# Kernel tuning notes

Measured on AMD Instinct MI355X. Metric: run time of the kernel, lower is better.

Reference implementation:

```python
import jax, jax.numpy as jnp
import numpy as np

B, T, D, H = 8, 1024, 1024, 16
HD = D // H  # head_dim = 64


def setup_inputs() -> dict:
    key = jax.random.key(0)
    ks = jax.random.split(key, 3)
    scale = 0.02
    return {
        "x": jax.random.normal(ks[0], (B, T, D), dtype=jnp.float32),
        "w_qkv": jax.random.normal(ks[1], (D, 3 * D), dtype=jnp.float32) * scale,
        "b_qkv": jnp.zeros((3 * D,), dtype=jnp.float32),
        "w_proj": jax.random.normal(ks[2], (D, D), dtype=jnp.float32) * scale,
        "b_proj": jnp.zeros((D,), dtype=jnp.float32),
    }


def reference(x, w_qkv, b_qkv, w_proj, b_proj):
    b, t, c = x.shape
    qkv = x @ w_qkv + b_qkv                      # [B,T,3D]
    qkv = qkv.reshape(b, t, 3, H, HD)
    q, k, v = [jnp.transpose(qkv[:, :, i], (0, 2, 1, 3)) for i in range(3)]  # [B,H,T,HD]
    att = jnp.einsum("bhqd,bhkd->bhqk", q, k) / np.sqrt(HD)
    causal = jnp.triu(jnp.ones((t, t), dtype=bool), k=1)
    att = jnp.where(causal, -jnp.inf, att)
    att = jax.nn.softmax(att, axis=-1)
    out = jnp.einsum("bhqk,bhkd->bhqd", att, v)  # [B,H,T,HD]
    out = jnp.transpose(out, (0, 2, 1, 3)).reshape(b, t, c)
    return out @ w_proj + b_proj
```

## Files before the change

### kernel.cpp

```cpp
#include <hip/hip_runtime.h>
#include <hip/hip_bf16.h>

#define BATCH 8
#define SEQ   1024
#define DIM   1024
#define NH    16
#define HDIM  64
#define LDQKV 3072

typedef __attribute__((ext_vector_type(8))) short bf16x8;
typedef __attribute__((ext_vector_type(4))) float f32x4;

typedef const __attribute__((address_space(1))) void* gvptr;
typedef __attribute__((address_space(3))) void* lvptr;

static __device__ __forceinline__ short f2bf(float f) {
    unsigned u = __float_as_uint(f);
    unsigned r = (u + 0x7fffu + ((u >> 16) & 1u)) >> 16;
    return (short)r;
}
static __device__ __forceinline__ unsigned pack2bf(float lo, float hi) {
    unsigned a = __float_as_uint(lo), b = __float_as_uint(hi);
    return ((a + 0x8000u) >> 16) | ((b + 0x8000u) & 0xffff0000u);
}

__global__ __launch_bounds__(256) void cast_f2b_kernel(
    const float* __restrict__ in, short* __restrict__ out)
{
    size_t i = ((size_t)blockIdx.x * 256 + threadIdx.x) * 8;
    float4 a = *(const float4*)&in[i];
    float4 b = *(const float4*)&in[i + 4];
    bf16x8 o;
    o[0] = f2bf(a.x); o[1] = f2bf(a.y); o[2] = f2bf(a.z); o[3] = f2bf(a.w);
    o[4] = f2bf(b.x); o[5] = f2bf(b.y); o[6] = f2bf(b.z); o[7] = f2bf(b.w);
    *(bf16x8*)&out[i] = o;
}

__global__ __launch_bounds__(256) void tcast_kernel(
    const float* __restrict__ in, short* __restrict__ out, int R, int C)
{
    __shared__ float Ld[32][33];
    const int tx = threadIdx.x & 31;
    const int ty = threadIdx.x >> 5;
    const int c0 = blockIdx.x * 32;
    const int r0 = blockIdx.y * 32;
#pragma unroll
    for (int i = 0; i < 4; i++) {
        int r = ty + i * 8;
        Ld[r][tx] = in[(size_t)(r0 + r) * C + c0 + tx];
    }
    __syncthreads();
#pragma unroll
    for (int i = 0; i < 4; i++) {
        int rr = ty + i * 8;
        out[(size_t)(c0 + rr) * R + r0 + tx] = f2bf(Ld[tx][rr]);
    }
}

#define GBM 128
#define GBN 256
#define GBK 64
#define NKT (DIM / GBK)
#define SLOT_SH (GBM * GBK + GBN * GBK)

static __device__ __forceinline__ void stage_tile(
    const short* __restrict__ A, const short* __restrict__ Bt,
    short* sb, int m0, int n0, int kt, int tid)
{
#pragma unroll
    for (int r = 0; r < 2; r++) {
        int off16 = tid + r * 512;
        int row   = off16 >> 3;
        int s     = (off16 & 7) ^ (row & 7);
        __builtin_amdgcn_global_load_lds(
            (gvptr)&A[(size_t)(m0 + row) * DIM + kt + s * 8],
            (lvptr)&sb[off16 * 8], 16, 0, 0);
    }
    short* bb = sb + GBM * GBK;
#pragma unroll
    for (int r = 0; r < 4; r++) {
        int off16 = tid + r * 512;
        int row   = off16 >> 3;
        int s     = (off16 & 7) ^ (row & 7);
        __builtin_amdgcn_global_load_lds(
            (gvptr)&Bt[(size_t)(n0 + row) * DIM + kt + s * 8],
            (lvptr)&bb[off16 * 8], 16, 0, 0);
    }
}

template<bool OUT_BF16>
__global__ __launch_bounds__(512, 2) void gemm_pipe_kernel(
    const short* __restrict__ A,
    const short* __restrict__ Bt,
    const float* __restrict__ bias,
    void* __restrict__ Cout,
    int N)
{
    __shared__ __align__(16) short lds[3 * SLOT_SH];

    const int tid  = threadIdx.x;
    const int lane = tid & 63;
    const int l16  = lane & 15;
    const int quad = lane >> 4;
    const int w    = tid >> 6;
    const int wm   = w >> 2;
    const int wn   = w & 3;
    const int m0   = blockIdx.y * GBM;
    const int n0   = blockIdx.x * GBN;

    f32x4 acc[4][4];
#pragma unroll
    for (int mi = 0; mi < 4; mi++)
#pragma unroll
        for (int ni = 0; ni < 4; ni++) acc[mi][ni] = (f32x4){0.f, 0.f, 0.f, 0.f};

    stage_tile(A, Bt, &lds[0],         m0, n0, 0,   tid);
    stage_tile(A, Bt, &lds[SLOT_SH],   m0, n0, GBK, tid);
    asm volatile("s_waitcnt vmcnt(6) lgkmcnt(0)\n\ts_barrier" ::: "memory");

#pragma unroll
    for (int t = 0; t < NKT; t++) {
        if (t + 2 < NKT)
            stage_tile(A, Bt, &lds[((t + 2) % 3) * SLOT_SH],
                       m0, n0, (t + 2) * GBK, tid);

        const short* ab = &lds[(t % 3) * SLOT_SH];
        const short* bb = ab + GBM * GBK;

        bf16x8 af[4][2], bfr[4][2];
#pragma unroll
        for (int mi = 0; mi < 4; mi++) {
            int row = wm * 64 + mi * 16 + l16;
#pragma unroll
            for (int ks = 0; ks < 2; ks++)
                af[mi][ks] = *(const bf16x8*)
                    &ab[row * GBK + (((ks * 4 + quad) ^ (row & 7)) * 8)];
        }
#pragma unroll
        for (int ni = 0; ni < 4; ni++) {
            int row = wn * 64 + ni * 16 + l16;
#pragma unroll
            for (int ks = 0; ks < 2; ks++)
                bfr[ni][ks] = *(const bf16x8*)
                    &bb[row * GBK + (((ks * 4 + quad) ^ (row & 7)) * 8)];
        }

        __builtin_amdgcn_s_setprio(1);
#pragma unroll
        for (int ks = 0; ks < 2; ks++)
#pragma unroll
            for (int mi = 0; mi < 4; mi++)
#pragma unroll
                for (int ni = 0; ni < 4; ni++)
                    acc[mi][ni] = __builtin_amdgcn_mfma_f32_16x16x32_bf16(
                        af[mi][ks], bfr[ni][ks], acc[mi][ni], 0, 0, 0);
        __builtin_amdgcn_s_setprio(0);

        if (t < NKT - 2)
            asm volatile("s_waitcnt vmcnt(6) lgkmcnt(0)\n\ts_barrier" ::: "memory");
        else if (t < NKT - 1)
            asm volatile("s_waitcnt vmcnt(0) lgkmcnt(0)\n\ts_barrier" ::: "memory");
    }

#pragma unroll
    for (int ni = 0; ni < 4; ni++) {
        int n = n0 + wn * 64 + ni * 16 + l16;
        float bv = bias[n];
#pragma unroll
        for (int mi = 0; mi < 4; mi++) {
#pragma unroll
            for (int reg = 0; reg < 4; reg++) {
                int m = m0 + wm * 64 + mi * 16 + quad * 4 + reg;
                float v = acc[mi][ni][reg] + bv;
                if (OUT_BF16)
                    ((short*)Cout)[(size_t)m * N + n] = f2bf(v);
                else
                    ((float*)Cout)[(size_t)m * N + n] = v;
            }
        }
    }
}

#define LDK 72
#define LDP 72

__global__ __launch_bounds__(256, 4) void attn_kernel(
    const short* __restrict__ qkv, short* __restrict__ out)
{
    const int bh    = blockIdx.x;
    const int qtile = 7 - (int)blockIdx.y;
    const int b  = bh >> 4;
    const int h  = bh & 15;
    const int q0 = qtile * 128;
    const int tid  = threadIdx.x;
    const int w    = tid >> 6;
    const int lane = tid & 63;
    const int l16  = lane & 15;
    const int quad = lane >> 4;

    __shared__ __align__(16) short Ks[64 * LDK];
    __shared__ __align__(16) short Vt[64 * LDK];
    __shared__ __align__(16) short QP[128 * LDP];

    const short* qbase = qkv + (size_t)(b * SEQ + q0) * LDQKV + h * HDIM;
#pragma unroll
    for (int s = 0; s < 4; s++) {
        int vi = tid + s * 256;
        int row = vi >> 3, d8 = (vi & 7) * 8;
        *(bf16x8*)&QP[row * LDP + d8] =
            *(const bf16x8*)&qbase[(size_t)row * LDQKV + d8];
    }
    __syncthreads();

    bf16x8 qfragT[2][2];
#pragma unroll
    for (int qb = 0; qb < 2; qb++)
#pragma unroll
        for (int ks = 0; ks < 2; ks++)
            qfragT[qb][ks] = *(const bf16x8*)
                &QP[(w * 32 + qb * 16 + l16) * LDP + ks * 32 + quad * 8];

    f32x4 o_accT[2][4];
#pragma unroll
    for (int qb = 0; qb < 2; qb++)
#pragma unroll
        for (int db = 0; db < 4; db++) o_accT[qb][db] = (f32x4){0.f, 0.f, 0.f, 0.f};
    float l_run[2] = {0.f, 0.f};

    const int nkt = 2 * qtile + 2;
    const short* kb0 = qkv + (size_t)b * SEQ * LDQKV + DIM + h * HDIM;
    const short* vb0 = kb0 + DIM;

    const int vkey0 = (tid & 15) * 4;
    const int vd4   = (tid >> 4) * 4;

    bf16x8 kreg[2];
    short4 vreg[4];
#pragma unroll
    for (int s = 0; s < 2; s++) {
        int vi = tid + s * 256;
        kreg[s] = *(const bf16x8*)&kb0[(size_t)(vi >> 3) * LDQKV + (vi & 7) * 8];
    }
#pragma unroll
    for (int i = 0; i < 4; i++)
        vreg[i] = *(const short4*)&vb0[(size_t)(vkey0 + i) * LDQKV + vd4];
#pragma unroll
    for (int s = 0; s < 2; s++) {
        int vi = tid + s * 256;
        *(bf16x8*)&Ks[(vi >> 3) * LDK + (vi & 7) * 8] = kreg[s];
    }
    *(short4*)&Vt[(vd4 + 0) * LDK + vkey0] = make_short4(vreg[0].x, vreg[1].x, vreg[2].x, vreg[3].x);
    *(short4*)&Vt[(vd4 + 1) * LDK + vkey0] = make_short4(vreg[0].y, vreg[1].y, vreg[2].y, vreg[3].y);
    *(short4*)&Vt[(vd4 + 2) * LDK + vkey0] = make_short4(vreg[0].z, vreg[1].z, vreg[2].z, vreg[3].z);
    *(short4*)&Vt[(vd4 + 3) * LDK + vkey0] = make_short4(vreg[0].w, vreg[1].w, vreg[2].w, vreg[3].w);

    for (int kt = 0; kt < nkt; kt++) {
        __syncthreads();
        const int k0 = kt * 64;

        if (kt + 1 < nkt) {
            const short* kb = kb0 + (size_t)(k0 + 64) * LDQKV;
            const short* vb = vb0 + (size_t)(k0 + 64) * LDQKV;
#pragma unroll
            for (int s = 0; s < 2; s++) {
                int vi = tid + s * 256;
                kreg[s] = *(const bf16x8*)&kb[(size_t)(vi >> 3) * LDQKV + (vi & 7) * 8];
            }
#pragma unroll
            for (int i = 0; i < 4; i++)
                vreg[i] = *(const short4*)&vb[(size_t)(vkey0 + i) * LDQKV + vd4];
        }

        f32x4 sT[2][4];
#pragma unroll
        for (int qb = 0; qb < 2; qb++)
#pragma unroll
            for (int kb = 0; kb < 4; kb++) sT[qb][kb] = (f32x4){0.f, 0.f, 0.f, 0.f};
#pragma unroll
        for (int kb = 0; kb < 4; kb++) {
            bf16x8 kf0 = *(const bf16x8*)&Ks[(kb * 16 + l16) * LDK + quad * 8];
            bf16x8 kf1 = *(const bf16x8*)&Ks[(kb * 16 + l16) * LDK + 32 + quad * 8];
#pragma unroll
            for (int qb = 0; qb < 2; qb++) {
                sT[qb][kb] = __builtin_amdgcn_mfma_f32_16x16x32_bf16(
                    kf0, qfragT[qb][0], sT[qb][kb], 0, 0, 0);
                sT[qb][kb] = __builtin_amdgcn_mfma_f32_16x16x32_bf16(
                    kf1, qfragT[qb][1], sT[qb][kb], 0, 0, 0);
            }
        }

        const bool domask = (kt >= nkt - 2);
#pragma unroll
        for (int qb = 0; qb < 2; qb++) {
            const int q = q0 + w * 32 + qb * 16 + l16;
            float lsum = 0.f;
#pragma unroll
            for (int kb = 0; kb < 4; kb++) {
                float p[4];
#pragma unroll
                for (int r = 0; r < 4; r++) {
                    float e = __expf(sT[qb][kb][r] * 0.125f);
                    int key = k0 + kb * 16 + quad * 4 + r;
                    p[r] = (!domask || key <= q) ? e : 0.f;
                    lsum += p[r];
                }
                unsigned d0 = pack2bf(p[0], p[1]);
                unsigned d1 = pack2bf(p[2], p[3]);
                *(uint2*)&QP[(w * 32 + qb * 16 + l16) * LDP + kb * 16 + quad * 4] =
                    make_uint2(d0, d1);
            }
            lsum += __shfl_xor(lsum, 16, 64);
            lsum += __shfl_xor(lsum, 32, 64);
            l_run[qb] += lsum;
        }

#pragma unroll
        for (int ks2 = 0; ks2 < 2; ks2++) {
            bf16x8 pf[2];
#pragma unroll
            for (int qb = 0; qb < 2; qb++)
                pf[qb] = *(const bf16x8*)
                    &QP[(w * 32 + qb * 16 + l16) * LDP + ks2 * 32 + quad * 8];
#pragma unroll
            for (int db = 0; db < 4; db++) {
                bf16x8 vf = *(const bf16x8*)&Vt[(db * 16 + l16) * LDK + ks2 * 32 + quad * 8];
#pragma unroll
                for (int qb = 0; qb < 2; qb++)
                    o_accT[qb][db] = __builtin_amdgcn_mfma_f32_16x16x32_bf16(
                        vf, pf[qb], o_accT[qb][db], 0, 0, 0);
            }
        }

        __syncthreads();
        if (kt + 1 < nkt) {
#pragma unroll
            for (int s = 0; s < 2; s++) {
                int vi = tid + s * 256;
                *(bf16x8*)&Ks[(vi >> 3) * LDK + (vi & 7) * 8] = kreg[s];
            }
            *(short4*)&Vt[(vd4 + 0) * LDK + vkey0] = make_short4(vreg[0].x, vreg[1].x, vreg[2].x, vreg[3].x);
            *(short4*)&Vt[(vd4 + 1) * LDK + vkey0] = make_short4(vreg[0].y, vreg[1].y, vreg[2].y, vreg[3].y);
            *(short4*)&Vt[(vd4 + 2) * LDK + vkey0] = make_short4(vreg[0].z, vreg[1].z, vreg[2].z, vreg[3].z);
            *(short4*)&Vt[(vd4 + 3) * LDK + vkey0] = make_short4(vreg[0].w, vreg[1].w, vreg[2].w, vreg[3].w);
        }
    }

#pragma unroll
    for (int qb = 0; qb < 2; qb++) {
        const float inv = 1.f / l_run[qb];
        const int q = q0 + w * 32 + qb * 16 + l16;
        short* ob = out + (size_t)(b * SEQ + q) * DIM + h * HDIM;
#pragma unroll
        for (int db = 0; db < 4; db++) {
            float v0 = o_accT[qb][db][0] * inv;
            float v1 = o_accT[qb][db][1] * inv;
            float v2 = o_accT[qb][db][2] * inv;
            float v3 = o_accT[qb][db][3] * inv;
            *(uint2*)&ob[db * 16 + quad * 4] =
                make_uint2(pack2bf(v0, v1), pack2bf(v2, v3));
        }
    }
}

extern "C" void kernel_launch(void* const* d_in, const int* in_sizes, int n_in,
                              void* d_out, int out_size, void* d_ws, size_t ws_size,
                              hipStream_t stream)
{
    const float* x      = (const float*)d_in[0];
    const float* w_qkv  = (const float*)d_in[1];
    const float* b_qkv  = (const float*)d_in[2];
    const float* w_proj = (const float*)d_in[3];
    const float* b_proj = (const float*)d_in[4];
    float* out = (float*)d_out;

    const int M = BATCH * SEQ;

    short* xb    = (short*)d_ws;
    short* wqb   = xb   + (size_t)M * DIM;
    short* wpb   = wqb  + (size_t)LDQKV * DIM;
    short* qkvb  = wpb  + (size_t)DIM * DIM;
    short* attnb = qkvb + (size_t)M * LDQKV;

    cast_f2b_kernel<<<(M * DIM) / (256 * 8), 256, 0, stream>>>(x, xb);
    tcast_kernel<<<dim3(LDQKV / 32, DIM / 32), 256, 0, stream>>>(w_qkv, wqb, DIM, LDQKV);
    tcast_kernel<<<dim3(DIM / 32, DIM / 32), 256, 0, stream>>>(w_proj, wpb, DIM, DIM);

    gemm_pipe_kernel<true><<<dim3(LDQKV / GBN, M / GBM), 512, 0, stream>>>(
        xb, wqb, b_qkv, (void*)qkvb, LDQKV);

    attn_kernel<<<dim3(BATCH * NH, SEQ / 128), 256, 0, stream>>>(qkvb, attnb);

    gemm_pipe_kernel<false><<<dim3(DIM / GBN, M / GBM), 512, 0, stream>>>(
        attnb, wpb, b_proj, (void*)out, DIM);
}
```

Measured before the change: 219.6 us.

## Replace triple-buffered GEMM with double-buffered 256-row tiles and per-GEMM N widths

The GEMM kernel moves from 128x256 tiles with a three-slot LDS pipeline to 256xBN tiles with two LDS buffers and plain __syncthreads between phases. The QKV projection uses BN=192 (16x32=512 blocks) and the output projection uses BN=128 (8x32=256 blocks), each warp now holding 8xNFR accumulators. The aim is more operand reuse per LDS load and better grid sizing for each GEMM. In exchange it adds register pressure (up to 8x3 f32x4 accumulators plus fragments) and drops the finer vmcnt-based overlap, relying on coarser barriers.

After: 224.0 us. +2.0%, slower.

```diff
diff --git a/kernel.cpp b/kernel.cpp
--- a/kernel.cpp
+++ b/kernel.cpp
@@ -57,46 +57,45 @@
     }
 }
 
-#define GBM 128
-#define GBN 256
-#define GBK 64
-#define NKT (DIM / GBK)
-#define SLOT_SH (GBM * GBK + GBN * GBK)
-
-static __device__ __forceinline__ void stage_tile(
+#define GK 1024
+
+template<int BN>
+static __device__ __forceinline__ void stage_tile_db(
     const short* __restrict__ A, const short* __restrict__ Bt,
     short* sb, int m0, int n0, int kt, int tid)
 {
-#pragma unroll
-    for (int r = 0; r < 2; r++) {
-        int off16 = tid + r * 512;
-        int row   = off16 >> 3;
-        int s     = (off16 & 7) ^ (row & 7);
-        __builtin_amdgcn_global_load_lds(
-            (gvptr)&A[(size_t)(m0 + row) * DIM + kt + s * 8],
-            (lvptr)&sb[off16 * 8], 16, 0, 0);
-    }
-    short* bb = sb + GBM * GBK;
 #pragma unroll
     for (int r = 0; r < 4; r++) {
         int off16 = tid + r * 512;
         int row   = off16 >> 3;
         int s     = (off16 & 7) ^ (row & 7);
         __builtin_amdgcn_global_load_lds(
-            (gvptr)&Bt[(size_t)(n0 + row) * DIM + kt + s * 8],
+            (gvptr)&A[(size_t)(m0 + row) * GK + kt + s * 8],
+            (lvptr)&sb[off16 * 8], 16, 0, 0);
+    }
+    short* bb = sb + 256 * 64;
+#pragma unroll
+    for (int r = 0; r < BN / 64; r++) {
+        int off16 = tid + r * 512;
+        int row   = off16 >> 3;
+        int s     = (off16 & 7) ^ (row & 7);
+        __builtin_amdgcn_global_load_lds(
+            (gvptr)&Bt[(size_t)(n0 + row) * GK + kt + s * 8],
             (lvptr)&bb[off16 * 8], 16, 0, 0);
     }
 }
 
-template<bool OUT_BF16>
-__global__ __launch_bounds__(512, 2) void gemm_pipe_kernel(
+template<int BN, bool OUT_BF16>
+__global__ __launch_bounds__(512, 2) void gemm_db_kernel(
     const short* __restrict__ A,
     const short* __restrict__ Bt,
     const float* __restrict__ bias,
     void* __restrict__ Cout,
     int N)
 {
-    __shared__ __align__(16) short lds[3 * SLOT_SH];
+    constexpr int NFR  = BN / 64;
+    constexpr int SLOT = 256 * 64 + BN * 64;
+    __shared__ __align__(16) short lds[2 * SLOT];
 
     const int tid  = threadIdx.x;
     const int lane = tid & 63;
@@ -105,72 +104,96 @@
     const int w    = tid >> 6;
     const int wm   = w >> 2;
     const int wn   = w & 3;
-    const int m0   = blockIdx.y * GBM;
-    const int n0   = blockIdx.x * GBN;
-
-    f32x4 acc[4][4];
-#pragma unroll
-    for (int mi = 0; mi < 4; mi++)
-#pragma unroll
-        for (int ni = 0; ni < 4; ni++) acc[mi][ni] = (f32x4){0.f, 0.f, 0.f, 0.f};
-
-    stage_tile(A, Bt, &lds[0],         m0, n0, 0,   tid);
-    stage_tile(A, Bt, &lds[SLOT_SH],   m0, n0, GBK, tid);
-    asm volatile("s_waitcnt vmcnt(6) lgkmcnt(0)\n\ts_barrier" ::: "memory");
-
-#pragma unroll
-    for (int t = 0; t < NKT; t++) {
-        if (t + 2 < NKT)
-            stage_tile(A, Bt, &lds[((t + 2) % 3) * SLOT_SH],
-                       m0, n0, (t + 2) * GBK, tid);
-
-        const short* ab = &lds[(t % 3) * SLOT_SH];
-        const short* bb = ab + GBM * GBK;
-
-        bf16x8 af[4][2], bfr[4][2];
-#pragma unroll
-        for (int mi = 0; mi < 4; mi++) {
-            int row = wm * 64 + mi * 16 + l16;
-#pragma unroll
-            for (int ks = 0; ks < 2; ks++)
-                af[mi][ks] = *(const bf16x8*)
-                    &ab[row * GBK + (((ks * 4 + quad) ^ (row & 7)) * 8)];
-        }
-#pragma unroll
-        for (int ni = 0; ni < 4; ni++) {
-            int row = wn * 64 + ni * 16 + l16;
-#pragma unroll
-            for (int ks = 0; ks < 2; ks++)
-                bfr[ni][ks] = *(const bf16x8*)
-                    &bb[row * GBK + (((ks * 4 + quad) ^ (row & 7)) * 8)];
-        }
-
-        __builtin_amdgcn_s_setprio(1);
-#pragma unroll
-        for (int ks = 0; ks < 2; ks++)
-#pragma unroll
-            for (int mi = 0; mi < 4; mi++)
-#pragma unroll
-                for (int ni = 0; ni < 4; ni++)
-                    acc[mi][ni] = __builtin_amdgcn_mfma_f32_16x16x32_bf16(
-                        af[mi][ks], bfr[ni][ks], acc[mi][ni], 0, 0, 0);
-        __builtin_amdgcn_s_setprio(0);
-
-        if (t < NKT - 2)
-            asm volatile("s_waitcnt vmcnt(6) lgkmcnt(0)\n\ts_barrier" ::: "memory");
-        else if (t < NKT - 1)
-            asm volatile("s_waitcnt vmcnt(0) lgkmcnt(0)\n\ts_barrier" ::: "memory");
-    }
-
-#pragma unroll
-    for (int ni = 0; ni < 4; ni++) {
-        int n = n0 + wn * 64 + ni * 16 + l16;
+    const int m0   = blockIdx.y * 256;
+    const int n0   = blockIdx.x * BN;
+
+    f32x4 acc[8][NFR];
+#pragma unroll
+    for (int mi = 0; mi < 8; mi++)
+#pragma unroll
+        for (int ni = 0; ni < NFR; ni++) acc[mi][ni] = (f32x4){0.f, 0.f, 0.f, 0.f};
+
+    stage_tile_db<BN>(A, Bt, &lds[0], m0, n0, 0, tid);
+    __syncthreads();
+
+    for (int t2 = 0; t2 < 8; t2++) {
+        const int ta = 2 * t2;
+        const int tb = 2 * t2 + 1;
+
+        stage_tile_db<BN>(A, Bt, &lds[SLOT], m0, n0, (ta + 1) * 64, tid);
+        {
+            const short* ab = &lds[0];
+            const short* bb = ab + 256 * 64;
+#pragma unroll
+            for (int ks = 0; ks < 2; ks++) {
+                bf16x8 af[8], bfr[NFR];
+#pragma unroll
+                for (int mi = 0; mi < 8; mi++) {
+                    int row = wm * 128 + mi * 16 + l16;
+                    af[mi] = *(const bf16x8*)
+                        &ab[row * 64 + (((ks * 4 + quad) ^ (row & 7)) * 8)];
+                }
+#pragma unroll
+                for (int ni = 0; ni < NFR; ni++) {
+                    int row = wn * (BN / 4) + ni * 16 + l16;
+                    bfr[ni] = *(const bf16x8*)
+                        &bb[row * 64 + (((ks * 4 + quad) ^ (row & 7)) * 8)];
+                }
+                __builtin_amdgcn_s_setprio(1);
+#pragma unroll
+                for (int mi = 0; mi < 8; mi++)
+#pragma unroll
+                    for (int ni = 0; ni < NFR; ni++)
+                        acc[mi][ni] = __builtin_amdgcn_mfma_f32_16x16x32_bf16(
+                            af[mi], bfr[ni], acc[mi][ni], 0, 0, 0);
+                __builtin_amdgcn_s_setprio(0);
+            }
+        }
+        __syncthreads();
+
+        if (t2 < 7)
+            stage_tile_db<BN>(A, Bt, &lds[0], m0, n0, (tb + 1) * 64, tid);
+        {
+            const short* ab = &lds[SLOT];
+            const short* bb = ab + 256 * 64;
+#pragma unroll
+            for (int ks = 0; ks < 2; ks++) {
+                bf16x8 af[8], bfr[NFR];
+#pragma unroll
+                for (int mi = 0; mi < 8; mi++) {
+                    int row = wm * 128 + mi * 16 + l16;
+                    af[mi] = *(const bf16x8*)
+                        &ab[row * 64 + (((ks * 4 + quad) ^ (row & 7)) * 8)];
+                }
+#pragma unroll
+                for (int ni = 0; ni < NFR; ni++) {
+                    int row = wn * (BN / 4) + ni * 16 + l16;
+                    bfr[ni] = *(const bf16x8*)
+                        &bb[row * 64 + (((ks * 4 + quad) ^ (row & 7)) * 8)];
+                }
+                __builtin_amdgcn_s_setprio(1);
+#pragma unroll
+                for (int mi = 0; mi < 8; mi++)
+#pragma unroll
+                    for (int ni = 0; ni < NFR; ni++)
+                        acc[mi][ni] = __builtin_amdgcn_mfma_f32_16x16x32_bf16(
+                            af[mi], bfr[ni], acc[mi][ni], 0, 0, 0);
+                __builtin_amdgcn_s_setprio(0);
+            }
+        }
+        if (t2 < 7)
+            __syncthreads();
+    }
+
+#pragma unroll
+    for (int ni = 0; ni < NFR; ni++) {
+        int n = n0 + wn * (BN / 4) + ni * 16 + l16;
         float bv = bias[n];
 #pragma unroll
-        for (int mi = 0; mi < 4; mi++) {
+        for (int mi = 0; mi < 8; mi++) {
 #pragma unroll
             for (int reg = 0; reg < 4; reg++) {
-                int m = m0 + wm * 64 + mi * 16 + quad * 4 + reg;
+                int m = m0 + wm * 128 + mi * 16 + quad * 4 + reg;
                 float v = acc[mi][ni][reg] + bv;
                 if (OUT_BF16)
                     ((short*)Cout)[(size_t)m * N + n] = f2bf(v);
@@ -385,11 +408,11 @@
     tcast_kernel<<<dim3(LDQKV / 32, DIM / 32), 256, 0, stream>>>(w_qkv, wqb, DIM, LDQKV);
     tcast_kernel<<<dim3(DIM / 32, DIM / 32), 256, 0, stream>>>(w_proj, wpb, DIM, DIM);
 
-    gemm_pipe_kernel<true><<<dim3(LDQKV / GBN, M / GBM), 512, 0, stream>>>(
+    gemm_db_kernel<192, true><<<dim3(LDQKV / 192, M / 256), 512, 0, stream>>>(
         xb, wqb, b_qkv, (void*)qkvb, LDQKV);
 
     attn_kernel<<<dim3(BATCH * NH, SEQ / 128), 256, 0, stream>>>(qkvb, attnb);
 
-    gemm_pipe_kernel<false><<<dim3(DIM / GBN, M / GBM), 512, 0, stream>>>(
+    gemm_db_kernel<128, false><<<dim3(DIM / 128, M / 256), 512, 0, stream>>>(
         attnb, wpb, b_proj, (void*)out, DIM);
 }
```

## Split GEMM k-step into two half-phases interleaving A/B staging with MFMA

Applied to the files above, without the earlier changes.

Restructures the GEMM main loop into two sub-phases per k-tile. Each phase loads half the fragments (ks=0 then ks=1), issues the A or B global-to-LDS staging for tile t+2, then runs MFMAs between extra barriers. The intent is to overlap global loads and LDS reads with matrix math more finely, in the style of a ping-pong schedule. The cost is more barriers per iteration, and the split of vmcnt accounting between A and B loads needs to stay correct.

New measurement: 220.1 us. Within noise of the previous version (+0.2%).

```diff
diff --git a/kernel.cpp b/kernel.cpp
--- a/kernel.cpp
+++ b/kernel.cpp
@@ -60,12 +60,12 @@
 #define GBM 128
 #define GBN 256
 #define GBK 64
-#define NKT (DIM / GBK)
+#define GK  1024
+#define NKT (GK / GBK)
 #define SLOT_SH (GBM * GBK + GBN * GBK)
 
-static __device__ __forceinline__ void stage_tile(
-    const short* __restrict__ A, const short* __restrict__ Bt,
-    short* sb, int m0, int n0, int kt, int tid)
+static __device__ __forceinline__ void stage_A(
+    const short* __restrict__ A, short* sb, int m0, int kt, int tid)
 {
 #pragma unroll
     for (int r = 0; r < 2; r++) {
@@ -73,18 +73,22 @@
         int row   = off16 >> 3;
         int s     = (off16 & 7) ^ (row & 7);
         __builtin_amdgcn_global_load_lds(
-            (gvptr)&A[(size_t)(m0 + row) * DIM + kt + s * 8],
+            (gvptr)&A[(size_t)(m0 + row) * GK + kt + s * 8],
             (lvptr)&sb[off16 * 8], 16, 0, 0);
     }
-    short* bb = sb + GBM * GBK;
+}
+
+static __device__ __forceinline__ void stage_B(
+    const short* __restrict__ Bt, short* bbuf, int n0, int kt, int tid)
+{
 #pragma unroll
     for (int r = 0; r < 4; r++) {
         int off16 = tid + r * 512;
         int row   = off16 >> 3;
         int s     = (off16 & 7) ^ (row & 7);
         __builtin_amdgcn_global_load_lds(
-            (gvptr)&Bt[(size_t)(n0 + row) * DIM + kt + s * 8],
-            (lvptr)&bb[off16 * 8], 16, 0, 0);
+            (gvptr)&Bt[(size_t)(n0 + row) * GK + kt + s * 8],
+            (lvptr)&bbuf[off16 * 8], 16, 0, 0);
     }
 }
 
@@ -114,52 +118,75 @@
 #pragma unroll
         for (int ni = 0; ni < 4; ni++) acc[mi][ni] = (f32x4){0.f, 0.f, 0.f, 0.f};
 
-    stage_tile(A, Bt, &lds[0],         m0, n0, 0,   tid);
-    stage_tile(A, Bt, &lds[SLOT_SH],   m0, n0, GBK, tid);
-    asm volatile("s_waitcnt vmcnt(6) lgkmcnt(0)\n\ts_barrier" ::: "memory");
+    stage_A(A, &lds[0], m0, 0, tid);
+    stage_B(Bt, &lds[0] + GBM * GBK, n0, 0, tid);
+    stage_A(A, &lds[SLOT_SH], m0, GBK, tid);
+    stage_B(Bt, &lds[SLOT_SH] + GBM * GBK, n0, GBK, tid);
+    asm volatile("s_waitcnt vmcnt(6) lgkmcnt(0)" ::: "memory");
+    __builtin_amdgcn_s_barrier();
 
 #pragma unroll
     for (int t = 0; t < NKT; t++) {
-        if (t + 2 < NKT)
-            stage_tile(A, Bt, &lds[((t + 2) % 3) * SLOT_SH],
-                       m0, n0, (t + 2) * GBK, tid);
-
         const short* ab = &lds[(t % 3) * SLOT_SH];
         const short* bb = ab + GBM * GBK;
-
-        bf16x8 af[4][2], bfr[4][2];
+        short* sb = &lds[((t + 2) % 3) * SLOT_SH];
+        const int kt2 = (t + 2) * GBK;
+
+        bf16x8 af0[4], bf0[4];
 #pragma unroll
         for (int mi = 0; mi < 4; mi++) {
             int row = wm * 64 + mi * 16 + l16;
-#pragma unroll
-            for (int ks = 0; ks < 2; ks++)
-                af[mi][ks] = *(const bf16x8*)
-                    &ab[row * GBK + (((ks * 4 + quad) ^ (row & 7)) * 8)];
+            af0[mi] = *(const bf16x8*)
+                &ab[row * GBK + ((quad ^ (row & 7)) * 8)];
         }
 #pragma unroll
         for (int ni = 0; ni < 4; ni++) {
             int row = wn * 64 + ni * 16 + l16;
-#pragma unroll
-            for (int ks = 0; ks < 2; ks++)
-                bfr[ni][ks] = *(const bf16x8*)
-                    &bb[row * GBK + (((ks * 4 + quad) ^ (row & 7)) * 8)];
-        }
-
+            bf0[ni] = *(const bf16x8*)
+                &bb[row * GBK + ((quad ^ (row & 7)) * 8)];
+        }
+        if (t + 2 < NKT) stage_A(A, sb, m0, kt2, tid);
+        __builtin_amdgcn_s_barrier();
+        asm volatile("s_waitcnt lgkmcnt(0)" ::: "memory");
         __builtin_amdgcn_s_setprio(1);
 #pragma unroll
-        for (int ks = 0; ks < 2; ks++)
-#pragma unroll
-            for (int mi = 0; mi < 4; mi++)
-#pragma unroll
-                for (int ni = 0; ni < 4; ni++)
-                    acc[mi][ni] = __builtin_amdgcn_mfma_f32_16x16x32_bf16(
-                        af[mi][ks], bfr[ni][ks], acc[mi][ni], 0, 0, 0);
+        for (int mi = 0; mi < 4; mi++)
+#pragma unroll
+            for (int ni = 0; ni < 4; ni++)
+                acc[mi][ni] = __builtin_amdgcn_mfma_f32_16x16x32_bf16(
+                    af0[mi], bf0[ni], acc[mi][ni], 0, 0, 0);
         __builtin_amdgcn_s_setprio(0);
-
+        __builtin_amdgcn_s_barrier();
+
+        bf16x8 af1[4], bf1[4];
+#pragma unroll
+        for (int mi = 0; mi < 4; mi++) {
+            int row = wm * 64 + mi * 16 + l16;
+            af1[mi] = *(const bf16x8*)
+                &ab[row * GBK + (((4 + quad) ^ (row & 7)) * 8)];
+        }
+#pragma unroll
+        for (int ni = 0; ni < 4; ni++) {
+            int row = wn * 64 + ni * 16 + l16;
+            bf1[ni] = *(const bf16x8*)
+                &bb[row * GBK + (((4 + quad) ^ (row & 7)) * 8)];
+        }
+        if (t + 2 < NKT) stage_B(Bt, sb + GBM * GBK, n0, kt2, tid);
+        __builtin_amdgcn_s_barrier();
+        asm volatile("s_waitcnt lgkmcnt(0)" ::: "memory");
+        __builtin_amdgcn_s_setprio(1);
+#pragma unroll
+        for (int mi = 0; mi < 4; mi++)
+#pragma unroll
+            for (int ni = 0; ni < 4; ni++)
+                acc[mi][ni] = __builtin_amdgcn_mfma_f32_16x16x32_bf16(
+                    af1[mi], bf1[ni], acc[mi][ni], 0, 0, 0);
+        __builtin_amdgcn_s_setprio(0);
         if (t < NKT - 2)
-            asm volatile("s_waitcnt vmcnt(6) lgkmcnt(0)\n\ts_barrier" ::: "memory");
+            asm volatile("s_waitcnt vmcnt(6)" ::: "memory");
         else if (t < NKT - 1)
-            asm volatile("s_waitcnt vmcnt(0) lgkmcnt(0)\n\ts_barrier" ::: "memory");
+            asm volatile("s_waitcnt vmcnt(0)" ::: "memory");
+        __builtin_amdgcn_s_barrier();
     }
 
 #pragma unroll
```
